# Performance work log

Hardware: AMD Instinct MI355X
Metric: run time of the kernel (lower is better)

Reference implementation:

```python
import jax, jax.numpy as jnp
import numpy as np

B, N, M, DIN, H = 8, 2048, 2048, 512, 256
SCALE = float(np.sqrt(H))


def _lin_params(key, din, dout):
    kw, kb = jax.random.split(key)
    lim = 1.0 / np.sqrt(din)
    W = jax.random.uniform(kw, (din, dout), jnp.float32, -lim, lim)
    b = jax.random.uniform(kb, (dout,), jnp.float32, -lim, lim)
    return W, b


def setup_inputs() -> dict:
    key = jax.random.key(0)
    ks = jax.random.split(key, 16)
    inp = {
        "q_fp": jax.random.normal(ks[0], (B, N, DIN), jnp.float32),
        "v_ret": jax.random.normal(ks[1], (B, M, DIN), jnp.float32),
        "pi_star": jax.random.uniform(ks[2], (B, N, M), jnp.float32),
    }
    names = ["qs", "ks", "vs", "qe", "ke", "ve"]
    for i, nm in enumerate(names):
        W, b = _lin_params(ks[3 + i], DIN, H)
        inp[f"W{nm}"], inp[f"b{nm}"] = W, b
    inp["W1"], inp["b1"] = _lin_params(ks[10], 4 * H, H)
    inp["W2"], inp["b2"] = _lin_params(ks[11], H, H)
    inp["gamma"] = jnp.ones((1,), jnp.float32)
    inp["ew"] = jnp.array(1.0, jnp.float32)
    return inp


def _forward(q_fp, v_ret, pi_star, Wqs, bqs, Wks, bks, Wvs, bvs,
             Wqe, bqe, Wke, bke, Wve, bve, W1, b1, W2, b2, gamma, ew):
    q_struct = q_fp @ Wqs + bqs          # [B,N,H]
    k_struct = v_ret @ Wks + bks         # [B,M,H]
    v_struct = v_ret @ Wvs + bvs
    q_elec = q_fp @ Wqe + bqe
    k_elec = v_ret @ Wke + bke
    v_elec = v_ret @ Wve + bve

    structural_logits = jnp.einsum("bnh,bmh->bnm", q_struct, k_struct) / SCALE

    # cdist(p=2) via the quadratic expansion, clamped for numeric safety
    q2 = jnp.sum(q_elec * q_elec, -1, keepdims=True)          # [B,N,1]
    k2 = jnp.sum(k_elec * k_elec, -1, keepdims=True)          # [B,M,1]
    d2 = q2 + jnp.swapaxes(k2, -2, -1) - 2.0 * jnp.einsum("bnh,bmh->bnm", q_elec, k_elec)
    electronic_distance = jnp.sqrt(jnp.maximum(d2, 1e-12))    # [B,N,M]
    electronic_scale = jnp.maximum(
        electronic_distance.mean(axis=(-2, -1), keepdims=True), 1e-4)
    electronic_logits = -(electronic_distance / electronic_scale)

    pi_mask = gamma * jnp.log(jnp.maximum(pi_star, 1e-9))
    final_logits = structural_logits + ew * electronic_logits + pi_mask
    attn = jax.nn.softmax(final_logits, axis=-1)              # [B,N,M]

    ctx_s = jnp.einsum("bnm,bmh->bnh", attn, v_struct)
    ctx_e = jnp.einsum("bnm,bmh->bnh", attn, v_elec)
    fused = jnp.concatenate([ctx_s, ctx_e, ctx_s - ctx_e, ctx_s * ctx_e], axis=-1)
    h = jax.nn.silu(fused @ W1 + b1)
    return h @ W2 + b2


def reference(q_fp, v_ret, pi_star, Wqs, bqs, Wks, bks, Wvs, bvs,
              Wqe, bqe, Wke, bke, Wve, bve, W1, b1, W2, b2, gamma, ew):
    return _forward(q_fp, v_ret, pi_star, Wqs, bqs, Wks, bks, Wvs, bvs,
                    Wqe, bqe, Wke, bke, Wve, bve, W1, b1, W2, b2, gamma, ew)
```

## Files before the change

### kernel.cpp

```cpp
#include <hip/hip_runtime.h>

#define Bsz 8
#define Nq  2048
#define Mk  2048
#define DINv 512
#define Hd  256
#define RQ  (Bsz*Nq)
#define RK  (Bsz*Mk)
#define BKt 32

typedef __attribute__((ext_vector_type(8))) short   short8;
typedef __attribute__((ext_vector_type(4))) float   floatx4;

__device__ __forceinline__ unsigned short f2bf(float f) {
  union { float f; unsigned u; } x; x.f = f;
  unsigned r = x.u + 0x7fffu + ((x.u >> 16) & 1u);
  return (unsigned short)(r >> 16);
}
__device__ __forceinline__ float bf2f(unsigned short s) {
  union { unsigned u; float f; } x; x.u = ((unsigned)s) << 16;
  return x.f;
}

__device__ __forceinline__ void gemm_core_nt(
    const unsigned short* __restrict__ A, int lda,
    const unsigned short* __restrict__ B, int ldb,
    int K, unsigned short* ldsA, unsigned short* ldsB,
    floatx4 (&acc)[4][4])
{
  const int tid  = threadIdx.x;
  const int lane = tid & 63;
  const int sr   = tid >> 2;
  const int sc   = (tid & 3) << 3;
  const int wid  = tid >> 6;
  const int wm   = wid & 1;
  const int wn   = wid >> 1;
  const int fr   = lane & 15;
  const int fk   = (lane >> 4) << 3;

  const unsigned short* a0p = A + (size_t)sr * lda + sc;
  const unsigned short* a1p = A + (size_t)(sr + 64) * lda + sc;
  const unsigned short* b0p = B + (size_t)sr * ldb + sc;
  const unsigned short* b1p = B + (size_t)(sr + 64) * ldb + sc;
  uint4* sa0 = (uint4*)(ldsA + sr * BKt + sc);
  uint4* sa1 = (uint4*)(ldsA + (sr + 64) * BKt + sc);
  uint4* sb0 = (uint4*)(ldsB + sr * BKt + sc);
  uint4* sb1 = (uint4*)(ldsB + (sr + 64) * BKt + sc);
  const unsigned short* fa = ldsA + (wm * 64 + fr) * BKt + fk;
  const unsigned short* fb = ldsB + (wn * 64 + fr) * BKt + fk;

  for (int k0 = 0; k0 < K; k0 += BKt) {
    uint4 a0 = *(const uint4*)a0p; a0p += BKt;
    uint4 a1 = *(const uint4*)a1p; a1p += BKt;
    uint4 b0 = *(const uint4*)b0p; b0p += BKt;
    uint4 b1 = *(const uint4*)b1p; b1p += BKt;
    __syncthreads();
    *sa0 = a0; *sa1 = a1; *sb0 = b0; *sb1 = b1;
    __syncthreads();
    short8 af[4], bf[4];
#pragma unroll
    for (int i = 0; i < 4; i++) af[i] = *(const short8*)(fa + i * 16 * BKt);
#pragma unroll
    for (int i = 0; i < 4; i++) bf[i] = *(const short8*)(fb + i * 16 * BKt);
#pragma unroll
    for (int i = 0; i < 4; i++)
#pragma unroll
      for (int j = 0; j < 4; j++)
        acc[i][j] = __builtin_amdgcn_mfma_f32_16x16x32_bf16(af[i], bf[j], acc[i][j], 0, 0, 0);
  }
}

#define EPILOGUE_VARS \
  const int lane = threadIdx.x & 63; \
  const int wid  = threadIdx.x >> 6; \
  const int wm   = wid & 1; \
  const int wn   = wid >> 1; \
  const int r4   = (lane >> 4) * 4;  \
  const int cn   = lane & 15;

template<int MODE>
__global__ __launch_bounds__(256) void k_gemm_bias(
    const unsigned short* __restrict__ A, const unsigned short* __restrict__ Bw,
    const float* __restrict__ bias, void* __restrict__ Cout, int Ncols, int K)
{
  __shared__ alignas(16) unsigned short ldsA[128 * BKt];
  __shared__ alignas(16) unsigned short ldsB[128 * BKt];
  floatx4 acc[4][4];
#pragma unroll
  for (int i = 0; i < 4; i++)
#pragma unroll
    for (int j = 0; j < 4; j++)
#pragma unroll
      for (int t = 0; t < 4; t++) acc[i][j][t] = 0.f;

  const unsigned short* Ab = A + (size_t)blockIdx.x * 128 * K;
  const unsigned short* Bb = Bw + (size_t)blockIdx.y * 128 * K;
  gemm_core_nt(Ab, K, Bb, K, K, ldsA, ldsB, acc);

  EPILOGUE_VARS
#pragma unroll
  for (int i = 0; i < 4; i++) {
#pragma unroll
    for (int j = 0; j < 4; j++) {
      int gc = blockIdx.y * 128 + wn * 64 + j * 16 + cn;
      float bv = bias[gc];
#pragma unroll
      for (int r = 0; r < 4; r++) {
        int gr = blockIdx.x * 128 + wm * 64 + i * 16 + r4 + r;
        float v = acc[i][j][r] + bv;
        if constexpr (MODE == 1) v = v / (1.f + __expf(-v));
        if constexpr (MODE == 2)
          ((float*)Cout)[(size_t)gr * Ncols + gc] = v;
        else
          ((unsigned short*)Cout)[(size_t)gr * Ncols + gc] = f2bf(v);
      }
    }
  }
}

__global__ __launch_bounds__(256) void k_pass1(
    const unsigned short* __restrict__ Xq, const unsigned short* __restrict__ Xk,
    const float* __restrict__ q2, const float* __restrict__ k2, float* __restrict__ dsum)
{
  __shared__ alignas(16) unsigned short ldsA[128 * BKt];
  __shared__ alignas(16) unsigned short ldsB[128 * BKt];
  floatx4 acc[4][4];
#pragma unroll
  for (int i = 0; i < 4; i++)
#pragma unroll
    for (int j = 0; j < 4; j++)
#pragma unroll
      for (int t = 0; t < 4; t++) acc[i][j][t] = 0.f;

  const int b = blockIdx.z;
  const unsigned short* Ab = Xq + ((size_t)(b * Nq) + blockIdx.x * 128) * 512 + 256;
  const unsigned short* Bb = Xk + ((size_t)(b * Mk) + blockIdx.y * 128) * 1024 + 512;
  gemm_core_nt(Ab, 512, Bb, 1024, 256, ldsA, ldsB, acc);

  EPILOGUE_VARS
  const int rowBase = b * Nq + blockIdx.x * 128;
  const int colBase = b * Mk + blockIdx.y * 128;
  float lsum = 0.f;
#pragma unroll
  for (int i = 0; i < 4; i++) {
#pragma unroll
    for (int j = 0; j < 4; j++) {
      float kk = k2[colBase + wn * 64 + j * 16 + cn];
#pragma unroll
      for (int r = 0; r < 4; r++) {
        float qq = q2[rowBase + wm * 64 + i * 16 + r4 + r];
        float d2 = qq + kk - 2.f * acc[i][j][r];
        lsum += sqrtf(fmaxf(d2, 1e-12f));
      }
    }
  }
#pragma unroll
  for (int o = 32; o; o >>= 1) lsum += __shfl_down(lsum, o);
  __syncthreads();
  float* red = (float*)ldsA;
  if (lane == 0) red[wid] = lsum;
  __syncthreads();
  if (threadIdx.x == 0) atomicAdd(dsum + b, red[0] + red[1] + red[2] + red[3]);
}

__global__ __launch_bounds__(256) void k_logits(
    const unsigned short* __restrict__ Xq, const unsigned short* __restrict__ Xk,
    const float* __restrict__ q2, const float* __restrict__ k2,
    const float* __restrict__ dsum, const float* __restrict__ pi,
    const float* __restrict__ gamma_p, const float* __restrict__ ew_p,
    _Float16* __restrict__ S)
{
  __shared__ alignas(16) unsigned short ldsA[128 * BKt];
  __shared__ alignas(16) unsigned short ldsB[128 * BKt];
  floatx4 accS[4][4], accE[4][4];
#pragma unroll
  for (int i = 0; i < 4; i++)
#pragma unroll
    for (int j = 0; j < 4; j++)
#pragma unroll
      for (int t = 0; t < 4; t++) { accS[i][j][t] = 0.f; accE[i][j][t] = 0.f; }

  const int b = blockIdx.z;
  const unsigned short* Aq_s = Xq + ((size_t)(b * Nq) + blockIdx.x * 128) * 512;
  const unsigned short* Bk_s = Xk + ((size_t)(b * Mk) + blockIdx.y * 128) * 1024;
  gemm_core_nt(Aq_s,       512, Bk_s,       1024, 256, ldsA, ldsB, accS);
  gemm_core_nt(Aq_s + 256, 512, Bk_s + 512, 1024, 256, ldsA, ldsB, accE);

  const float scale = fmaxf(dsum[b] * (1.f / (2048.f * 2048.f)), 1e-4f);
  const float einv  = ew_p[0] / scale;
  const float gv    = gamma_p[0];

  EPILOGUE_VARS
#pragma unroll
  for (int i = 0; i < 4; i++) {
#pragma unroll
    for (int j = 0; j < 4; j++) {
      int m = blockIdx.y * 128 + wn * 64 + j * 16 + cn;
      float kk = k2[b * Mk + m];
#pragma unroll
      for (int r = 0; r < 4; r++) {
        int n = blockIdx.x * 128 + wm * 64 + i * 16 + r4 + r;
        float qq = q2[b * Nq + n];
        float d  = sqrtf(fmaxf(qq + kk - 2.f * accE[i][j][r], 1e-12f));
        float p  = pi[((size_t)b * Nq + n) * Mk + m];
        float l  = accS[i][j][r] * 0.0625f - einv * d + gv * __logf(fmaxf(p, 1e-9f));
        S[((size_t)b * Nq + n) * Mk + m] = (_Float16)l;
      }
    }
  }
}

__global__ __launch_bounds__(256) void k_softmax(
    const _Float16* __restrict__ S, unsigned short* __restrict__ W)
{
  __shared__ float red[8];
  const size_t rowoff = (size_t)blockIdx.x * Mk;
  const int t = threadIdx.x;
  union { uint4 u; _Float16 h[8]; } inb;
  inb.u = *(const uint4*)(S + rowoff + t * 8);
  float f[8];
  float mx = -1e30f;
#pragma unroll
  for (int i = 0; i < 8; i++) { f[i] = (float)inb.h[i]; mx = fmaxf(mx, f[i]); }
  const int lane = t & 63, wid = t >> 6;
#pragma unroll
  for (int o = 32; o; o >>= 1) mx = fmaxf(mx, __shfl_down(mx, o));
  if (lane == 0) red[wid] = mx;
  __syncthreads();
  mx = fmaxf(fmaxf(red[0], red[1]), fmaxf(red[2], red[3]));
  float s = 0.f;
#pragma unroll
  for (int i = 0; i < 8; i++) { f[i] = __expf(f[i] - mx); s += f[i]; }
#pragma unroll
  for (int o = 32; o; o >>= 1) s += __shfl_down(s, o);
  if (lane == 0) red[4 + wid] = s;
  __syncthreads();
  s = red[4] + red[5] + red[6] + red[7];
  const float rinv = 1.f / s;
  unsigned short os[8];
#pragma unroll
  for (int i = 0; i < 8; i++) os[i] = f2bf(f[i] * rinv);
  uint4 o4;
  o4.x = os[0] | ((unsigned)os[1] << 16);
  o4.y = os[2] | ((unsigned)os[3] << 16);
  o4.z = os[4] | ((unsigned)os[5] << 16);
  o4.w = os[6] | ((unsigned)os[7] << 16);
  *(uint4*)(W + rowoff + t * 8) = o4;
}

__global__ __launch_bounds__(256) void k_pv(
    const unsigned short* __restrict__ At, const unsigned short* __restrict__ VT,
    unsigned short* __restrict__ ctx)
{
  __shared__ alignas(16) unsigned short ldsA[128 * BKt];
  __shared__ alignas(16) unsigned short ldsB[128 * BKt];
  floatx4 acc[4][4];
#pragma unroll
  for (int i = 0; i < 4; i++)
#pragma unroll
    for (int j = 0; j < 4; j++)
#pragma unroll
      for (int t = 0; t < 4; t++) acc[i][j][t] = 0.f;

  const int b = blockIdx.z;
  const unsigned short* Ab = At + ((size_t)b * Nq + blockIdx.x * 128) * (size_t)Mk;
  const unsigned short* Bb = VT + ((size_t)b * 512 + blockIdx.y * 128) * (size_t)Mk;
  gemm_core_nt(Ab, Mk, Bb, Mk, Mk, ldsA, ldsB, acc);

  EPILOGUE_VARS
#pragma unroll
  for (int i = 0; i < 4; i++)
#pragma unroll
    for (int j = 0; j < 4; j++) {
      int gc = blockIdx.y * 128 + wn * 64 + j * 16 + cn;
#pragma unroll
      for (int r = 0; r < 4; r++) {
        int gr = blockIdx.x * 128 + wm * 64 + i * 16 + r4 + r;
        ctx[((size_t)b * Nq + gr) * 512 + gc] = f2bf(acc[i][j][r]);
      }
    }
}

__global__ void k_f32_bf16(const float* __restrict__ src, unsigned short* __restrict__ dst) {
  size_t i = ((size_t)blockIdx.x * 256 + threadIdx.x) * 4;
  float4 v = *(const float4*)(src + i);
  uint2 o;
  o.x = f2bf(v.x) | ((unsigned)f2bf(v.y) << 16);
  o.y = f2bf(v.z) | ((unsigned)f2bf(v.w) << 16);
  *(uint2*)(dst + i) = o;
}

__global__ void k_prep_w(
    const float* __restrict__ Wqs, const float* __restrict__ Wqe,
    const float* __restrict__ Wks, const float* __restrict__ Wvs,
    const float* __restrict__ Wke, const float* __restrict__ Wve,
    const float* __restrict__ W1,  const float* __restrict__ W2,
    const float* __restrict__ bqs, const float* __restrict__ bqe,
    const float* __restrict__ bks, const float* __restrict__ bvs,
    const float* __restrict__ bke, const float* __restrict__ bve,
    unsigned short* __restrict__ WqT, unsigned short* __restrict__ WkT,
    unsigned short* __restrict__ W1T, unsigned short* __restrict__ W2T,
    float* __restrict__ bq, float* __restrict__ bk, float* __restrict__ dsum)
{
  int gid = blockIdx.x * 256 + threadIdx.x;
  int idx = gid;
  if (idx < 512 * 512) {
    int j = idx >> 9, k = idx & 511;
    float v = (j < 256) ? Wqs[k * 256 + j] : Wqe[k * 256 + (j - 256)];
    WqT[idx] = f2bf(v);
  } else if ((idx -= 512 * 512) < 1024 * 512) {
    int j = idx >> 9, k = idx & 511;
    int s = j >> 8, jj = j & 255;
    const float* Wp = (s == 0) ? Wks : (s == 1) ? Wvs : (s == 2) ? Wke : Wve;
    WkT[idx] = f2bf(Wp[k * 256 + jj]);
  } else if ((idx -= 1024 * 512) < 256 * 1024) {
    int j = idx >> 10, k = idx & 1023;
    W1T[idx] = f2bf(W1[k * 256 + j]);
  } else if ((idx -= 256 * 1024) < 256 * 256) {
    int j = idx >> 8, k = idx & 255;
    W2T[idx] = f2bf(W2[k * 256 + j]);
  }
  if (gid < 512)  bq[gid] = (gid < 256) ? bqs[gid] : bqe[gid - 256];
  if (gid < 1024) bk[gid] = (gid < 256) ? bks[gid]
                    : (gid < 512) ? bvs[gid - 256]
                    : (gid < 768) ? bke[gid - 512] : bve[gid - 768];
  if (gid < 8) dsum[gid] = 0.f;
}

__global__ __launch_bounds__(256) void k_rowsq(
    const unsigned short* __restrict__ X, int stride, int colOff, float* __restrict__ out)
{
  int row = blockIdx.x * 4 + (threadIdx.x >> 6);
  int lane = threadIdx.x & 63;
  const unsigned short* p = X + (size_t)row * stride + colOff + lane * 4;
  uint2 u = *(const uint2*)p;
  float a0 = bf2f((unsigned short)(u.x & 0xffff));
  float a1 = bf2f((unsigned short)(u.x >> 16));
  float a2 = bf2f((unsigned short)(u.y & 0xffff));
  float a3 = bf2f((unsigned short)(u.y >> 16));
  float s = a0 * a0 + a1 * a1 + a2 * a2 + a3 * a3;
#pragma unroll
  for (int o = 32; o; o >>= 1) s += __shfl_down(s, o);
  if (lane == 0) out[row] = s;
}

__global__ void k_trans_vt(const unsigned short* __restrict__ Xk, unsigned short* __restrict__ VT) {
  __shared__ unsigned short t[32][33];
  const int b = blockIdx.z;
  const int m0 = blockIdx.x * 32, j0 = blockIdx.y * 32;
  const int tx = threadIdx.x, ty = threadIdx.y;
#pragma unroll
  for (int i = 0; i < 4; i++) {
    int m = m0 + ty + i * 8;
    int j = j0 + tx;
    int c = (j < 256) ? (256 + j) : (512 + j);
    t[ty + i * 8][tx] = Xk[((size_t)b * Mk + m) * 1024 + c];
  }
  __syncthreads();
#pragma unroll
  for (int i = 0; i < 4; i++) {
    int j = j0 + ty + i * 8;
    int m = m0 + tx;
    VT[((size_t)b * 512 + j) * Mk + m] = t[tx][ty + i * 8];
  }
}

__global__ void k_fused(const unsigned short* __restrict__ ctx, unsigned short* __restrict__ fused) {
  int idx = blockIdx.x * 256 + threadIdx.x;
  int bn = idx >> 8;
  int j = idx & 255;
  float cs = bf2f(ctx[(size_t)bn * 512 + j]);
  float ce = bf2f(ctx[(size_t)bn * 512 + 256 + j]);
  size_t o = (size_t)bn * 1024 + j;
  fused[o]       = f2bf(cs);
  fused[o + 256] = f2bf(ce);
  fused[o + 512] = f2bf(cs - ce);
  fused[o + 768] = f2bf(cs * ce);
}

extern "C" void kernel_launch(void* const* d_in, const int* in_sizes, int n_in,
                              void* d_out, int out_size, void* d_ws, size_t ws_size,
                              hipStream_t stream) {
  (void)in_sizes; (void)n_in; (void)out_size; (void)ws_size;
  const float* q_fp  = (const float*)d_in[0];
  const float* v_ret = (const float*)d_in[1];
  const float* pi    = (const float*)d_in[2];
  const float* Wqs = (const float*)d_in[3];  const float* bqs = (const float*)d_in[4];
  const float* Wks = (const float*)d_in[5];  const float* bks = (const float*)d_in[6];
  const float* Wvs = (const float*)d_in[7];  const float* bvs = (const float*)d_in[8];
  const float* Wqe = (const float*)d_in[9];  const float* bqe = (const float*)d_in[10];
  const float* Wke = (const float*)d_in[11]; const float* bke = (const float*)d_in[12];
  const float* Wve = (const float*)d_in[13]; const float* bve = (const float*)d_in[14];
  const float* W1  = (const float*)d_in[15]; const float* b1  = (const float*)d_in[16];
  const float* W2  = (const float*)d_in[17]; const float* b2  = (const float*)d_in[18];
  const float* gamma = (const float*)d_in[19];
  const float* ew    = (const float*)d_in[20];

  char* w = (char*)d_ws;
  unsigned short* WqT = (unsigned short*)(w + 0);
  unsigned short* WkT = (unsigned short*)(w + 524288);
  unsigned short* W1T = (unsigned short*)(w + 1572864);
  unsigned short* W2T = (unsigned short*)(w + 2097152);
  float* bq   = (float*)(w + 2228224);
  float* bk   = (float*)(w + 2230272);
  float* q2   = (float*)(w + 2234368);
  float* k2   = (float*)(w + 2299904);
  float* dsum = (float*)(w + 2365440);
  unsigned short* Aq = (unsigned short*)(w + 2365696);
  unsigned short* Ak = (unsigned short*)(w + 19142912);
  unsigned short* Xq = (unsigned short*)(w + 35920128);
  unsigned short* Xk = (unsigned short*)(w + 52697344);
  unsigned short* VT = (unsigned short*)(w + 86251776);
  _Float16*       S  = (_Float16*)(w + 103028992);
  unsigned short* attn = (unsigned short*)(w + 103028992);
  unsigned short* ctx  = Aq;
  unsigned short* fused = (unsigned short*)(w + 103028992);
  unsigned short* hbuf  = Ak;

  k_f32_bf16<<<8192, 256, 0, stream>>>(q_fp, Aq);
  k_f32_bf16<<<8192, 256, 0, stream>>>(v_ret, Ak);
  k_prep_w<<<4352, 256, 0, stream>>>(Wqs, Wqe, Wks, Wvs, Wke, Wve, W1, W2,
                                     bqs, bqe, bks, bvs, bke, bve,
                                     WqT, WkT, W1T, W2T, bq, bk, dsum);
  k_gemm_bias<0><<<dim3(128, 4), 256, 0, stream>>>(Aq, WqT, bq, Xq, 512, 512);
  k_gemm_bias<0><<<dim3(128, 8), 256, 0, stream>>>(Ak, WkT, bk, Xk, 1024, 512);
  k_rowsq<<<4096, 256, 0, stream>>>(Xq, 512, 256, q2);
  k_rowsq<<<4096, 256, 0, stream>>>(Xk, 1024, 512, k2);
  k_pass1<<<dim3(16, 16, 8), 256, 0, stream>>>(Xq, Xk, q2, k2, dsum);
  k_logits<<<dim3(16, 16, 8), 256, 0, stream>>>(Xq, Xk, q2, k2, dsum, pi, gamma, ew, S);
  k_softmax<<<16384, 256, 0, stream>>>(S, attn);
  k_trans_vt<<<dim3(64, 16, 8), dim3(32, 8), 0, stream>>>(Xk, VT);
  k_pv<<<dim3(16, 4, 8), 256, 0, stream>>>(attn, VT, ctx);
  k_fused<<<16384, 256, 0, stream>>>(ctx, fused);
  k_gemm_bias<1><<<dim3(128, 2), 256, 0, stream>>>(fused, W1T, b1, hbuf, 256, 1024);
  k_gemm_bias<2><<<dim3(128, 2), 256, 0, stream>>>(hbuf, W2T, b2, d_out, 256, 256);
}
```

Before: 598.3 us.

## Fuse softmax exponentiation into logits epilogue and defer normalization to PV

The separate softmax kernel is removed. The logits kernel now writes exp(logit) directly as bf16 and accumulates per-row sums with shuffles and atomics into a scratch buffer (aliased onto the output). The PV kernel then scales each context row by the reciprocal of its sum. This drops one full write and read of the B×N×M intermediate. It also drops the max-subtraction step, so it depends on logits staying in a range where exp does not overflow. Separately, the shared GEMM core now uses global_load_lds to copy tiles straight into LDS instead of staging them through registers.

```diff
diff --git a/kernel.cpp b/kernel.cpp
--- a/kernel.cpp
+++ b/kernel.cpp
@@ -3,10 +3,6 @@
 #define Bsz 8
 #define Nq  2048
 #define Mk  2048
-#define DINv 512
-#define Hd  256
-#define RQ  (Bsz*Nq)
-#define RK  (Bsz*Mk)
 #define BKt 32
 
 typedef __attribute__((ext_vector_type(8))) short   short8;
@@ -20,6 +16,12 @@
 __device__ __forceinline__ float bf2f(unsigned short s) {
   union { unsigned u; float f; } x; x.u = ((unsigned)s) << 16;
   return x.f;
+}
+
+__device__ __forceinline__ void async16(const unsigned short* g, unsigned short* l) {
+  __builtin_amdgcn_global_load_lds(
+      (const __attribute__((address_space(1))) unsigned int*)g,
+      (__attribute__((address_space(3))) unsigned int*)l, 16, 0, 0);
 }
 
 __device__ __forceinline__ void gemm_core_nt(
@@ -42,31 +44,30 @@
   const unsigned short* a1p = A + (size_t)(sr + 64) * lda + sc;
   const unsigned short* b0p = B + (size_t)sr * ldb + sc;
   const unsigned short* b1p = B + (size_t)(sr + 64) * ldb + sc;
-  uint4* sa0 = (uint4*)(ldsA + sr * BKt + sc);
-  uint4* sa1 = (uint4*)(ldsA + (sr + 64) * BKt + sc);
-  uint4* sb0 = (uint4*)(ldsB + sr * BKt + sc);
-  uint4* sb1 = (uint4*)(ldsB + (sr + 64) * BKt + sc);
+  unsigned short* la0 = ldsA + tid * 8;
+  unsigned short* la1 = ldsA + 2048 + tid * 8;
+  unsigned short* lb0 = ldsB + tid * 8;
+  unsigned short* lb1 = ldsB + 2048 + tid * 8;
   const unsigned short* fa = ldsA + (wm * 64 + fr) * BKt + fk;
   const unsigned short* fb = ldsB + (wn * 64 + fr) * BKt + fk;
 
   for (int k0 = 0; k0 < K; k0 += BKt) {
-    uint4 a0 = *(const uint4*)a0p; a0p += BKt;
-    uint4 a1 = *(const uint4*)a1p; a1p += BKt;
-    uint4 b0 = *(const uint4*)b0p; b0p += BKt;
-    uint4 b1 = *(const uint4*)b1p; b1p += BKt;
     __syncthreads();
-    *sa0 = a0; *sa1 = a1; *sb0 = b0; *sb1 = b1;
+    async16(a0p, la0); a0p += BKt;
+    async16(a1p, la1); a1p += BKt;
+    async16(b0p, lb0); b0p += BKt;
+    async16(b1p, lb1); b1p += BKt;
     __syncthreads();
-    short8 af[4], bf[4];
-#pragma unroll
-    for (int i = 0; i < 4; i++) af[i] = *(const short8*)(fa + i * 16 * BKt);
-#pragma unroll
-    for (int i = 0; i < 4; i++) bf[i] = *(const short8*)(fb + i * 16 * BKt);
+    short8 af[4], bfr[4];
+#pragma unroll
+    for (int i = 0; i < 4; i++) af[i]  = *(const short8*)(fa + i * 16 * BKt);
+#pragma unroll
+    for (int i = 0; i < 4; i++) bfr[i] = *(const short8*)(fb + i * 16 * BKt);
 #pragma unroll
     for (int i = 0; i < 4; i++)
 #pragma unroll
       for (int j = 0; j < 4; j++)
-        acc[i][j] = __builtin_amdgcn_mfma_f32_16x16x32_bf16(af[i], bf[j], acc[i][j], 0, 0, 0);
+        acc[i][j] = __builtin_amdgcn_mfma_f32_16x16x32_bf16(af[i], bfr[j], acc[i][j], 0, 0, 0);
   }
 }
 
@@ -76,7 +77,8 @@
   const int wm   = wid & 1; \
   const int wn   = wid >> 1; \
   const int r4   = (lane >> 4) * 4;  \
-  const int cn   = lane & 15;
+  const int cn   = lane & 15; \
+  (void)wid;
 
 template<int MODE>
 __global__ __launch_bounds__(256) void k_gemm_bias(
@@ -120,8 +122,13 @@
 
 __global__ __launch_bounds__(256) void k_pass1(
     const unsigned short* __restrict__ Xq, const unsigned short* __restrict__ Xk,
-    const float* __restrict__ q2, const float* __restrict__ k2, float* __restrict__ dsum)
-{
+    const float* __restrict__ q2, const float* __restrict__ k2,
+    float* __restrict__ dsum, float* __restrict__ rowsum)
+{
+  {
+    int blin = (blockIdx.z * 16 + blockIdx.y) * 16 + blockIdx.x;
+    if (threadIdx.x < 8) rowsum[blin * 8 + threadIdx.x] = 0.f;
+  }
   __shared__ alignas(16) unsigned short ldsA[128 * BKt];
   __shared__ alignas(16) unsigned short ldsB[128 * BKt];
   floatx4 acc[4][4];
@@ -168,7 +175,7 @@
     const float* __restrict__ q2, const float* __restrict__ k2,
     const float* __restrict__ dsum, const float* __restrict__ pi,
     const float* __restrict__ gamma_p, const float* __restrict__ ew_p,
-    _Float16* __restrict__ S)
+    unsigned short* __restrict__ attn, float* __restrict__ rowsum)
 {
   __shared__ alignas(16) unsigned short ldsA[128 * BKt];
   __shared__ alignas(16) unsigned short ldsB[128 * BKt];
@@ -191,6 +198,12 @@
   const float gv    = gamma_p[0];
 
   EPILOGUE_VARS
+  float rs[4][4];
+#pragma unroll
+  for (int i = 0; i < 4; i++)
+#pragma unroll
+    for (int r = 0; r < 4; r++) rs[i][r] = 0.f;
+
 #pragma unroll
   for (int i = 0; i < 4; i++) {
 #pragma unroll
@@ -204,53 +217,27 @@
         float d  = sqrtf(fmaxf(qq + kk - 2.f * accE[i][j][r], 1e-12f));
         float p  = pi[((size_t)b * Nq + n) * Mk + m];
         float l  = accS[i][j][r] * 0.0625f - einv * d + gv * __logf(fmaxf(p, 1e-9f));
-        S[((size_t)b * Nq + n) * Mk + m] = (_Float16)l;
+        float e  = __expf(l);
+        rs[i][r] += e;
+        attn[((size_t)b * Nq + n) * Mk + m] = f2bf(e);
       }
     }
   }
-}
-
-__global__ __launch_bounds__(256) void k_softmax(
-    const _Float16* __restrict__ S, unsigned short* __restrict__ W)
-{
-  __shared__ float red[8];
-  const size_t rowoff = (size_t)blockIdx.x * Mk;
-  const int t = threadIdx.x;
-  union { uint4 u; _Float16 h[8]; } inb;
-  inb.u = *(const uint4*)(S + rowoff + t * 8);
-  float f[8];
-  float mx = -1e30f;
-#pragma unroll
-  for (int i = 0; i < 8; i++) { f[i] = (float)inb.h[i]; mx = fmaxf(mx, f[i]); }
-  const int lane = t & 63, wid = t >> 6;
-#pragma unroll
-  for (int o = 32; o; o >>= 1) mx = fmaxf(mx, __shfl_down(mx, o));
-  if (lane == 0) red[wid] = mx;
-  __syncthreads();
-  mx = fmaxf(fmaxf(red[0], red[1]), fmaxf(red[2], red[3]));
-  float s = 0.f;
-#pragma unroll
-  for (int i = 0; i < 8; i++) { f[i] = __expf(f[i] - mx); s += f[i]; }
-#pragma unroll
-  for (int o = 32; o; o >>= 1) s += __shfl_down(s, o);
-  if (lane == 0) red[4 + wid] = s;
-  __syncthreads();
-  s = red[4] + red[5] + red[6] + red[7];
-  const float rinv = 1.f / s;
-  unsigned short os[8];
-#pragma unroll
-  for (int i = 0; i < 8; i++) os[i] = f2bf(f[i] * rinv);
-  uint4 o4;
-  o4.x = os[0] | ((unsigned)os[1] << 16);
-  o4.y = os[2] | ((unsigned)os[3] << 16);
-  o4.z = os[4] | ((unsigned)os[5] << 16);
-  o4.w = os[6] | ((unsigned)os[7] << 16);
-  *(uint4*)(W + rowoff + t * 8) = o4;
+#pragma unroll
+  for (int i = 0; i < 4; i++)
+#pragma unroll
+    for (int r = 0; r < 4; r++) {
+      float v = rs[i][r];
+      v += __shfl_xor(v, 1); v += __shfl_xor(v, 2);
+      v += __shfl_xor(v, 4); v += __shfl_xor(v, 8);
+      if (cn == 0)
+        atomicAdd(rowsum + b * Nq + blockIdx.x * 128 + wm * 64 + i * 16 + r4 + r, v);
+    }
 }
 
 __global__ __launch_bounds__(256) void k_pv(
     const unsigned short* __restrict__ At, const unsigned short* __restrict__ VT,
-    unsigned short* __restrict__ ctx)
+    const float* __restrict__ rowsum, unsigned short* __restrict__ ctx)
 {
   __shared__ alignas(16) unsigned short ldsA[128 * BKt];
   __shared__ alignas(16) unsigned short ldsB[128 * BKt];
@@ -268,6 +255,13 @@
   gemm_core_nt(Ab, Mk, Bb, Mk, Mk, ldsA, ldsB, acc);
 
   EPILOGUE_VARS
+  const int rowbase = b * Nq + blockIdx.x * 128 + wm * 64;
+  float rinv[4][4];
+#pragma unroll
+  for (int i = 0; i < 4; i++)
+#pragma unroll
+    for (int r = 0; r < 4; r++)
+      rinv[i][r] = 1.f / rowsum[rowbase + i * 16 + r4 + r];
 #pragma unroll
   for (int i = 0; i < 4; i++)
 #pragma unroll
@@ -276,7 +270,7 @@
 #pragma unroll
       for (int r = 0; r < 4; r++) {
         int gr = blockIdx.x * 128 + wm * 64 + i * 16 + r4 + r;
-        ctx[((size_t)b * Nq + gr) * 512 + gc] = f2bf(acc[i][j][r]);
+        ctx[((size_t)b * Nq + gr) * 512 + gc] = f2bf(acc[i][j][r] * rinv[i][r]);
       }
     }
 }
@@ -411,11 +405,11 @@
   unsigned short* Xq = (unsigned short*)(w + 35920128);
   unsigned short* Xk = (unsigned short*)(w + 52697344);
   unsigned short* VT = (unsigned short*)(w + 86251776);
-  _Float16*       S  = (_Float16*)(w + 103028992);
   unsigned short* attn = (unsigned short*)(w + 103028992);
   unsigned short* ctx  = Aq;
   unsigned short* fused = (unsigned short*)(w + 103028992);
   unsigned short* hbuf  = Ak;
+  float* rowsum = (float*)d_out;
 
   k_f32_bf16<<<8192, 256, 0, stream>>>(q_fp, Aq);
   k_f32_bf16<<<8192, 256, 0, stream>>>(v_ret, Ak);
@@ -426,11 +420,11 @@
   k_gemm_bias<0><<<dim3(128, 8), 256, 0, stream>>>(Ak, WkT, bk, Xk, 1024, 512);
   k_rowsq<<<4096, 256, 0, stream>>>(Xq, 512, 256, q2);
   k_rowsq<<<4096, 256, 0, stream>>>(Xk, 1024, 512, k2);
-  k_pass1<<<dim3(16, 16, 8), 256, 0, stream>>>(Xq, Xk, q2, k2, dsum);
-  k_logits<<<dim3(16, 16, 8), 256, 0, stream>>>(Xq, Xk, q2, k2, dsum, pi, gamma, ew, S);
-  k_softmax<<<16384, 256, 0, stream>>>(S, attn);
+  k_pass1<<<dim3(16, 16, 8), 256, 0, stream>>>(Xq, Xk, q2, k2, dsum, rowsum);
+  k_logits<<<dim3(16, 16, 8), 256, 0, stream>>>(Xq, Xk, q2, k2, dsum, pi, gamma, ew,
+                                                attn, rowsum);
   k_trans_vt<<<dim3(64, 16, 8), dim3(32, 8), 0, stream>>>(Xk, VT);
-  k_pv<<<dim3(16, 4, 8), 256, 0, stream>>>(attn, VT, ctx);
+  k_pv<<<dim3(16, 4, 8), 256, 0, stream>>>(attn, VT, rowsum, ctx);
   k_fused<<<16384, 256, 0, stream>>>(ctx, fused);
   k_gemm_bias<1><<<dim3(128, 2), 256, 0, stream>>>(fused, W1T, b1, hbuf, 256, 1024);
   k_gemm_bias<2><<<dim3(128, 2), 256, 0, stream>>>(hbuf, W2T, b2, d_out, 256, 256);
```

New measurement: 671.0 us. +12.2%, slower.
